# Performance work log

Hardware: AMD Instinct MI355X
Metric: run time of the kernel (lower is better)

The kernel has to match this reference:

```python
import jax, jax.numpy as jnp
import numpy as np

N, C, D, H, O = 8192, 100, 128, 128, 64


def setup_inputs() -> dict:
    key = jax.random.key(0)
    k1, k2, k3, k4 = jax.random.split(key, 4)
    x = jax.random.normal(k1, (N, D), dtype=jnp.float32)
    cat_ids = jax.random.randint(k2, (N,), 0, C)
    W1 = 0.02 * jax.random.normal(k3, (C, D, H), dtype=jnp.float32)
    b1 = jnp.zeros((C, H), dtype=jnp.float32)
    W2 = 0.02 * jax.random.normal(k4, (C, H, O), dtype=jnp.float32)
    b2 = jnp.zeros((C, O), dtype=jnp.float32)
    return {"x": x, "cat_ids": cat_ids, "W1": W1, "b1": b1, "W2": W2, "b2": b2}


def reference(x, cat_ids, W1, b1, W2, b2):
    # Layer 1: per-token category-weight gather + matmul + bias, then ReLU.
    # selected_W1: [N, D, H] (the large gathered intermediate, as in the torch code)
    h = jax.nn.relu(jnp.einsum('nd,ndh->nh', x, W1[cat_ids]) + b1[cat_ids])
    # Layer 2: [N, H] x [N, H, O] -> [N, O]
    out = jnp.einsum('nh,nho->no', h, W2[cat_ids]) + b2[cat_ids]
    return out
```

## Files before the change

kernel.cpp:

```cpp
#include <hip/hip_runtime.h>


#define N_TOK 8192
#define C_CAT 100
#define D_IN  128
#define H_MID 128
#define O_OUT 64
#define TPB   32
#define MAX_ITEMS (C_CAT + N_TOK / TPB)


#define COMP(v,k) ((k)==0?(v).x:((k)==1?(v).y:((k)==2?(v).z:(v).w)))

__global__ __launch_bounds__(1024) void prologue_kernel(
    const int* __restrict__ cat_ids, int* __restrict__ ws) {
  __shared__ int cnt[C_CAT];
  __shared__ int cur[C_CAT];
  __shared__ int sc[128], sk[128];
  int t = threadIdx.x;
  if (t < C_CAT) cnt[t] = 0;
  __syncthreads();

  int ids[8];
  #pragma unroll
  for (int k = 0; k < 8; ++k) {
    ids[k] = cat_ids[t + (k << 10)];
    atomicAdd(&cnt[ids[k]], 1);
  }
  __syncthreads();

  int v = 0, ck = 0;
  if (t < 128) {
    v  = (t < C_CAT) ? cnt[t] : 0;
    ck = (v + TPB - 1) / TPB;
    sc[t] = v; sk[t] = ck;
  }
  __syncthreads();
  for (int off = 1; off < 128; off <<= 1) {
    int a = 0, b = 0;
    if (t < 128 && t >= off) { a = sc[t - off]; b = sk[t - off]; }
    __syncthreads();
    if (t < 128) { sc[t] += a; sk[t] += b; }
    __syncthreads();
  }
  if (t < C_CAT) {
    int start = sc[t] - v;
    int ibase = sk[t] - ck;
    cur[t] = start;
    int* items = ws + 272;
    for (int k = 0; k < ck; ++k) {
      items[3 * (ibase + k) + 0] = t;
      items[3 * (ibase + k) + 1] = start + k * TPB;
      items[3 * (ibase + k) + 2] = min(TPB, v - k * TPB);
    }
  }
  if (t == 127) ws[256] = sk[127];
  __syncthreads();

  #pragma unroll
  for (int k = 0; k < 8; ++k) {
    int pos = atomicAdd(&cur[ids[k]], 1);
    ws[2048 + pos] = t + (k << 10);
  }
}

__global__ __launch_bounds__(256) void mlp_kernel(
    const float* __restrict__ x,  const float* __restrict__ W1,
    const float* __restrict__ b1, const float* __restrict__ W2,
    const float* __restrict__ b2, float* __restrict__ out,
    const int* __restrict__ ws) {
  int bid = blockIdx.x;
  if (bid >= ws[256]) return;
  const int* item = ws + 272 + 3 * bid;
  int cat = item[0], start = item[1], cnt = item[2];
  const int* sorted = ws + 2048;

  __shared__ float xh[TPB][132];
  __shared__ float w1t[32][128];
  __shared__ int   toks[TPB];

  int tid = threadIdx.x;
  if (tid < TPB) toks[tid] = (tid < cnt) ? sorted[start + tid] : sorted[start];
  __syncthreads();

  {
    int f4 = tid & 31;
    int r0 = tid >> 5;
    #pragma unroll
    for (int it = 0; it < 4; ++it) {
      int i = r0 + (it << 3);
      if (i < cnt) {
        float4 vv = ((const float4*)(x + (size_t)toks[i] * D_IN))[f4];
        *(float4*)&xh[i][f4 << 2] = vv;
      }
    }
  }

  int c0 = (tid >> 3) << 2;
  int tg = tid & 7;
  float4 acc[4];
  #pragma unroll
  for (int j = 0; j < 4; ++j) acc[j] = make_float4(0.f, 0.f, 0.f, 0.f);

  for (int dt = 0; dt < 4; ++dt) {
    __syncthreads();
    {
      int f4 = tid & 31;
      int r0 = tid >> 5;
      #pragma unroll
      for (int rr = 0; rr < 4; ++rr) {
        int r = r0 + (rr << 3);
        float4 vv = ((const float4*)(W1 + ((size_t)cat * D_IN + dt * 32 + r) * H_MID))[f4];
        *(float4*)&w1t[r][f4 << 2] = vv;
      }
    }
    __syncthreads();
    #pragma unroll
    for (int dq = 0; dq < 8; ++dq) {
      float4 xv[4];
      #pragma unroll
      for (int j = 0; j < 4; ++j)
        xv[j] = *(float4*)&xh[tg + (j << 3)][(dt << 5) + (dq << 2)];
      #pragma unroll
      for (int k = 0; k < 4; ++k) {
        float4 wv = *(float4*)&w1t[(dq << 2) + k][c0];
        #pragma unroll
        for (int j = 0; j < 4; ++j) {
          float xs = COMP(xv[j], k);
          acc[j].x = fmaf(xs, wv.x, acc[j].x);
          acc[j].y = fmaf(xs, wv.y, acc[j].y);
          acc[j].z = fmaf(xs, wv.z, acc[j].z);
          acc[j].w = fmaf(xs, wv.w, acc[j].w);
        }
      }
    }
  }

  float4 b1v = *(const float4*)(b1 + (size_t)cat * H_MID + c0);
  __syncthreads();
  #pragma unroll
  for (int j = 0; j < 4; ++j) {
    float4 hv;
    hv.x = fmaxf(acc[j].x + b1v.x, 0.f);
    hv.y = fmaxf(acc[j].y + b1v.y, 0.f);
    hv.z = fmaxf(acc[j].z + b1v.z, 0.f);
    hv.w = fmaxf(acc[j].w + b1v.w, 0.f);
    *(float4*)&xh[tg + (j << 3)][c0] = hv;
  }
  __syncthreads();

  int o0  = (tid >> 4) << 2;
  int tg2 = tid & 15;
  float4 acc2[2];
  acc2[0] = make_float4(0.f, 0.f, 0.f, 0.f);
  acc2[1] = make_float4(0.f, 0.f, 0.f, 0.f);

  #pragma unroll 4
  for (int hq = 0; hq < 32; ++hq) {
    float4 hv[2];
    hv[0] = *(float4*)&xh[tg2][hq << 2];
    hv[1] = *(float4*)&xh[tg2 + 16][hq << 2];
    #pragma unroll
    for (int k = 0; k < 4; ++k) {
      float4 wv = *(const float4*)(W2 + ((size_t)cat * H_MID + (hq << 2) + k) * O_OUT + o0);
      #pragma unroll
      for (int j = 0; j < 2; ++j) {
        float hs = COMP(hv[j], k);
        acc2[j].x = fmaf(hs, wv.x, acc2[j].x);
        acc2[j].y = fmaf(hs, wv.y, acc2[j].y);
        acc2[j].z = fmaf(hs, wv.z, acc2[j].z);
        acc2[j].w = fmaf(hs, wv.w, acc2[j].w);
      }
    }
  }

  float4 b2v = *(const float4*)(b2 + (size_t)cat * O_OUT + o0);
  #pragma unroll
  for (int j = 0; j < 2; ++j) {
    int tk = tg2 + (j << 4);
    if (tk < cnt) {
      float4 r;
      r.x = acc2[j].x + b2v.x;
      r.y = acc2[j].y + b2v.y;
      r.z = acc2[j].z + b2v.z;
      r.w = acc2[j].w + b2v.w;
      *(float4*)(out + (size_t)toks[tk] * O_OUT + o0) = r;
    }
  }
}

extern "C" void kernel_launch(void* const* d_in, const int* in_sizes, int n_in,
                              void* d_out, int out_size, void* d_ws, size_t ws_size,
                              hipStream_t stream) {
  const float* x       = (const float*)d_in[0];
  const int*   cat_ids = (const int*)  d_in[1];
  const float* W1      = (const float*)d_in[2];
  const float* b1      = (const float*)d_in[3];
  const float* W2      = (const float*)d_in[4];
  const float* b2      = (const float*)d_in[5];
  float* out = (float*)d_out;
  int*   ws  = (int*)d_ws;

  prologue_kernel<<<1, 1024, 0, stream>>>(cat_ids, ws);
  mlp_kernel<<<MAX_ITEMS, 256, 0, stream>>>(x, W1, b1, W2, b2, out, ws);
}
```

Before: 99.47 us.

## Map one token per lane and stream wave-uniform weights directly from global memory

Tokens per work item double to 64 and blocks grow to 512 threads, so each of eight waves owns a 16-column slice of the hidden layer and an 8-column slice of the output. Each lane handles one token. Weight rows are read with wave-uniform addresses straight from global/L1 instead of being staged through shared memory, which removes the W1 tile buffer and its barriers. Biases now initialise the accumulators. The cost is less register-level reuse of x per weight load, and partially filled items waste more lanes now that they hold 64 tokens.

After: 113.1 us. 13.8% more time.

```diff
diff --git a/kernel.cpp b/kernel.cpp
--- a/kernel.cpp
+++ b/kernel.cpp
@@ -6,7 +6,7 @@
 #define D_IN  128
 #define H_MID 128
 #define O_OUT 64
-#define TPB   32
+#define TPB   64
 #define MAX_ITEMS (C_CAT + N_TOK / TPB)
 
 
@@ -64,7 +64,7 @@
   }
 }
 
-__global__ __launch_bounds__(256) void mlp_kernel(
+__global__ __launch_bounds__(512) void mlp_kernel(
     const float* __restrict__ x,  const float* __restrict__ W1,
     const float* __restrict__ b1, const float* __restrict__ W2,
     const float* __restrict__ b2, float* __restrict__ out,
@@ -76,7 +76,6 @@
   const int* sorted = ws + 2048;
 
   __shared__ float xh[TPB][132];
-  __shared__ float w1t[32][128];
   __shared__ int   toks[TPB];
 
   int tid = threadIdx.x;
@@ -84,108 +83,84 @@
   __syncthreads();
 
   {
-    int f4 = tid & 31;
-    int r0 = tid >> 5;
+    int f4 = tid & 31, r0 = tid >> 5;
     #pragma unroll
-    for (int it = 0; it < 4; ++it) {
-      int i = r0 + (it << 3);
-      if (i < cnt) {
-        float4 vv = ((const float4*)(x + (size_t)toks[i] * D_IN))[f4];
-        *(float4*)&xh[i][f4 << 2] = vv;
+    for (int p = 0; p < 4; ++p) {
+      int r = r0 + (p << 4);
+      float4 v = ((const float4*)(x + (size_t)toks[r] * D_IN))[f4];
+      *(float4*)&xh[r][f4 << 2] = v;
+    }
+  }
+  __syncthreads();
+
+  int lane = tid & 63;
+  int wv = __builtin_amdgcn_readfirstlane(tid >> 6);
+
+  const float* W1c = W1 + (size_t)cat * (D_IN * H_MID) + (wv << 4);
+  const float* bb1 = b1 + (size_t)cat * H_MID + (wv << 4);
+  float4 a[4];
+  #pragma unroll
+  for (int q = 0; q < 4; ++q) a[q] = *(const float4*)(bb1 + (q << 2));
+
+  for (int d4 = 0; d4 < D_IN; d4 += 4) {
+    float4 xv = *(float4*)&xh[lane][d4];
+    #pragma unroll
+    for (int i = 0; i < 4; ++i) {
+      const float* wr = W1c + (size_t)(d4 + i) * H_MID;
+      float4 w[4];
+      #pragma unroll
+      for (int q = 0; q < 4; ++q) w[q] = ((const float4*)wr)[q];
+      float xs = COMP(xv, i);
+      #pragma unroll
+      for (int q = 0; q < 4; ++q) {
+        a[q].x = fmaf(xs, w[q].x, a[q].x);
+        a[q].y = fmaf(xs, w[q].y, a[q].y);
+        a[q].z = fmaf(xs, w[q].z, a[q].z);
+        a[q].w = fmaf(xs, w[q].w, a[q].w);
       }
     }
   }
 
-  int c0 = (tid >> 3) << 2;
-  int tg = tid & 7;
-  float4 acc[4];
+  __syncthreads();
   #pragma unroll
-  for (int j = 0; j < 4; ++j) acc[j] = make_float4(0.f, 0.f, 0.f, 0.f);
+  for (int q = 0; q < 4; ++q) {
+    float4 hv;
+    hv.x = fmaxf(a[q].x, 0.f);
+    hv.y = fmaxf(a[q].y, 0.f);
+    hv.z = fmaxf(a[q].z, 0.f);
+    hv.w = fmaxf(a[q].w, 0.f);
+    *(float4*)&xh[lane][(wv << 4) + (q << 2)] = hv;
+  }
+  __syncthreads();
 
-  for (int dt = 0; dt < 4; ++dt) {
-    __syncthreads();
-    {
-      int f4 = tid & 31;
-      int r0 = tid >> 5;
-      #pragma unroll
-      for (int rr = 0; rr < 4; ++rr) {
-        int r = r0 + (rr << 3);
-        float4 vv = ((const float4*)(W1 + ((size_t)cat * D_IN + dt * 32 + r) * H_MID))[f4];
-        *(float4*)&w1t[r][f4 << 2] = vv;
-      }
-    }
-    __syncthreads();
+  const float* W2c = W2 + (size_t)cat * (H_MID * O_OUT) + (wv << 3);
+  const float* bb2 = b2 + (size_t)cat * O_OUT + (wv << 3);
+  float4 c0 = *(const float4*)(bb2 + 0);
+  float4 c1 = *(const float4*)(bb2 + 4);
+
+  for (int h4 = 0; h4 < H_MID; h4 += 4) {
+    float4 hv = *(float4*)&xh[lane][h4];
     #pragma unroll
-    for (int dq = 0; dq < 8; ++dq) {
-      float4 xv[4];
-      #pragma unroll
-      for (int j = 0; j < 4; ++j)
-        xv[j] = *(float4*)&xh[tg + (j << 3)][(dt << 5) + (dq << 2)];
-      #pragma unroll
-      for (int k = 0; k < 4; ++k) {
-        float4 wv = *(float4*)&w1t[(dq << 2) + k][c0];
-        #pragma unroll
-        for (int j = 0; j < 4; ++j) {
-          float xs = COMP(xv[j], k);
-          acc[j].x = fmaf(xs, wv.x, acc[j].x);
-          acc[j].y = fmaf(xs, wv.y, acc[j].y);
-          acc[j].z = fmaf(xs, wv.z, acc[j].z);
-          acc[j].w = fmaf(xs, wv.w, acc[j].w);
-        }
-      }
+    for (int i = 0; i < 4; ++i) {
+      const float* wr = W2c + (size_t)(h4 + i) * O_OUT;
+      float4 w0 = ((const float4*)wr)[0];
+      float4 w1 = ((const float4*)wr)[1];
+      float hs = COMP(hv, i);
+      c0.x = fmaf(hs, w0.x, c0.x);
+      c0.y = fmaf(hs, w0.y, c0.y);
+      c0.z = fmaf(hs, w0.z, c0.z);
+      c0.w = fmaf(hs, w0.w, c0.w);
+      c1.x = fmaf(hs, w1.x, c1.x);
+      c1.y = fmaf(hs, w1.y, c1.y);
+      c1.z = fmaf(hs, w1.z, c1.z);
+      c1.w = fmaf(hs, w1.w, c1.w);
     }
   }
 
-  float4 b1v = *(const float4*)(b1 + (size_t)cat * H_MID + c0);
-  __syncthreads();
-  #pragma unroll
-  for (int j = 0; j < 4; ++j) {
-    float4 hv;
-    hv.x = fmaxf(acc[j].x + b1v.x, 0.f);
-    hv.y = fmaxf(acc[j].y + b1v.y, 0.f);
-    hv.z = fmaxf(acc[j].z + b1v.z, 0.f);
-    hv.w = fmaxf(acc[j].w + b1v.w, 0.f);
-    *(float4*)&xh[tg + (j << 3)][c0] = hv;
-  }
-  __syncthreads();
-
-  int o0  = (tid >> 4) << 2;
-  int tg2 = tid & 15;
-  float4 acc2[2];
-  acc2[0] = make_float4(0.f, 0.f, 0.f, 0.f);
-  acc2[1] = make_float4(0.f, 0.f, 0.f, 0.f);
-
-  #pragma unroll 4
-  for (int hq = 0; hq < 32; ++hq) {
-    float4 hv[2];
-    hv[0] = *(float4*)&xh[tg2][hq << 2];
-    hv[1] = *(float4*)&xh[tg2 + 16][hq << 2];
-    #pragma unroll
-    for (int k = 0; k < 4; ++k) {
-      float4 wv = *(const float4*)(W2 + ((size_t)cat * H_MID + (hq << 2) + k) * O_OUT + o0);
-      #pragma unroll
-      for (int j = 0; j < 2; ++j) {
-        float hs = COMP(hv[j], k);
-        acc2[j].x = fmaf(hs, wv.x, acc2[j].x);
-        acc2[j].y = fmaf(hs, wv.y, acc2[j].y);
-        acc2[j].z = fmaf(hs, wv.z, acc2[j].z);
-        acc2[j].w = fmaf(hs, wv.w, acc2[j].w);
-      }
-    }
-  }
-
-  float4 b2v = *(const float4*)(b2 + (size_t)cat * O_OUT + o0);
-  #pragma unroll
-  for (int j = 0; j < 2; ++j) {
-    int tk = tg2 + (j << 4);
-    if (tk < cnt) {
-      float4 r;
-      r.x = acc2[j].x + b2v.x;
-      r.y = acc2[j].y + b2v.y;
-      r.z = acc2[j].z + b2v.z;
-      r.w = acc2[j].w + b2v.w;
-      *(float4*)(out + (size_t)toks[tk] * O_OUT + o0) = r;
-    }
+  if (lane < cnt) {
+    float* op = out + (size_t)toks[lane] * O_OUT + (wv << 3);
+    *(float4*)(op + 0) = c0;
+    *(float4*)(op + 4) = c1;
   }
 }
 
@@ -202,5 +177,5 @@
   int*   ws  = (int*)d_ws;
 
   prologue_kernel<<<1, 1024, 0, stream>>>(cat_ids, ws);
-  mlp_kernel<<<MAX_ITEMS, 256, 0, stream>>>(x, W1, b1, W2, b2, out, ws);
+  mlp_kernel<<<MAX_ITEMS, 512, 0, stream>>>(x, W1, b1, W2, b2, out, ws);
 }
```
